# Kernel tuning notes

Measured on AMD Instinct MI355X. Metric: run time of the kernel, lower is better.

The kernel has to match this reference:

```python
import jax, jax.numpy as jnp
import numpy as np

N, L, D = 4, 2048, 1024
H_DIM, OUT_DIM = 1024, 1024


def setup_inputs() -> dict:
    key = jax.random.key(0)
    ks = jax.random.split(key, 7)
    scale = 0.02
    return {
        "x": jax.random.normal(ks[0], (N, L, D), dtype=jnp.float32),
        "Wq": jax.random.normal(ks[1], (D, H_DIM), dtype=jnp.float32) * scale,
        "bq": jnp.zeros((H_DIM,), dtype=jnp.float32),
        "Wk": jax.random.normal(ks[2], (D, H_DIM), dtype=jnp.float32) * scale,
        "bk": jnp.zeros((H_DIM,), dtype=jnp.float32),
        "Wv": jax.random.normal(ks[3], (D, OUT_DIM), dtype=jnp.float32) * scale,
        "bv": jnp.zeros((OUT_DIM,), dtype=jnp.float32),
    }


def reference(x, Wq, bq, Wk, bk, Wv, bv):
    # q,k: [N,L,h_dim], v: [N,L,out_dim]
    q = jnp.einsum("nld,dh->nlh", x, Wq) + bq
    k = jnp.einsum("nld,dh->nlh", x, Wk) + bk
    v = jnp.einsum("nld,do->nlo", x, Wv) + bv
    # scores: [N,L,L]
    qk = jnp.einsum("nlh,nmh->nlm", q, k)
    # NOTE: original scales by sqrt(qk.shape[-1]) == sqrt(L) (seq len), not sqrt(h_dim)
    seq_len = qk.shape[-1]
    s = jax.nn.softmax(qk / jnp.sqrt(jnp.asarray(seq_len, dtype=qk.dtype)), axis=-1)
    return jnp.einsum("nlm,nmo->nlo", s, v)
```

## Files before the change

### kernel.cpp

```cpp
#include <hip/hip_runtime.h>
#include <hip/hip_bf16.h>


typedef __attribute__((ext_vector_type(8))) short bf16x8;
typedef __attribute__((ext_vector_type(4))) float f32x4;

#define AS_G(p) ((__attribute__((address_space(1))) void*)(p))
#define AS_L(p) ((__attribute__((address_space(3))) void*)(p))

__device__ __forceinline__ unsigned short f2bf(float f) {
  unsigned int u = __float_as_uint(f);
  unsigned int lsb = (u >> 16) & 1u;
  u += 0x7fffu + lsb;
  return (unsigned short)(u >> 16);
}

#define WAITV(n) asm volatile("s_waitcnt vmcnt(" #n ")" ::: "memory")
#define BARRIER() do { asm volatile("" ::: "memory");                         \
    __builtin_amdgcn_s_barrier();                                             \
    asm volatile("" ::: "memory");                                            \
    __builtin_amdgcn_sched_barrier(0); } while (0)


#define S64A(ktk, rb, bofs)                                                   \
  __builtin_amdgcn_global_load_lds(                                           \
      AS_G(A + (size_t)(rowBase + (rb) * 64 + r0) * lda + (ktk) + goff),      \
      AS_L(lds + (bofs) + (rb) * 4096 + t * 8), 16, 0, 0)

#define S64B(ktk, rb, bofs)                                                   \
  __builtin_amdgcn_global_load_lds(                                           \
      AS_G(B + (size_t)(colBase + (rb) * 64 + r0) * ldb + (ktk) + goff),      \
      AS_L(lds + (bofs) + 16384 + (rb) * 4096 + t * 8), 16, 0, 0)

#define STAGE_TILE(ktk, bofs) do {                                            \
    S64A(ktk, 0, bofs); S64A(ktk, 1, bofs);                                   \
    S64A(ktk, 2, bofs); S64A(ktk, 3, bofs);                                   \
    S64B(ktk, 0, bofs); S64B(ktk, 1, bofs);                                   \
    S64B(ktk, 2, bofs); S64B(ktk, 3, bofs); } while (0)

#define LOAD_A(ih, bofs) do { _Pragma("unroll")                               \
    for (int ks_ = 0; ks_ < 2; ks_++) { _Pragma("unroll")                     \
      for (int ii = 0; ii < 4; ii++) {                                        \
        int row_ = wrow + ((ih) * 4 + ii) * 16 + r16;                         \
        int slot_ = (ks_ * 4 + q) ^ (r16 & 7);                                \
        af[ks_][ii] = *(const bf16x8*)(lds + (bofs) + row_ * 64 + slot_ * 8); \
      } } } while (0)

#define LOAD_B(jh, bofs) do { _Pragma("unroll")                               \
    for (int ks_ = 0; ks_ < 2; ks_++) { _Pragma("unroll")                     \
      for (int jj = 0; jj < 2; jj++) {                                        \
        int row_ = wcol + ((jh) * 2 + jj) * 16 + r16;                         \
        int slot_ = (ks_ * 4 + q) ^ (r16 & 7);                                \
        bfr[ks_][(jh) * 2 + jj] =                                             \
            *(const bf16x8*)(lds + (bofs) + 16384 + row_ * 64 + slot_ * 8);   \
      } } } while (0)

#define MM(ih, jh) do { __builtin_amdgcn_s_setprio(1); _Pragma("unroll")      \
    for (int ks_ = 0; ks_ < 2; ks_++) { _Pragma("unroll")                     \
      for (int ii = 0; ii < 4; ii++) { _Pragma("unroll")                      \
        for (int jj = 0; jj < 2; jj++)                                        \
          acc[(ih) * 4 + ii][(jh) * 2 + jj] =                                 \
              __builtin_amdgcn_mfma_f32_16x16x32_bf16(                        \
                  af[ks_][ii], bfr[ks_][(jh) * 2 + jj],                       \
                  acc[(ih) * 4 + ii][(jh) * 2 + jj], 0, 0, 0);                \
      } }                                                                     \
    __builtin_amdgcn_s_setprio(0); } while (0)

#define TILE(ktc, bofs, obofs) do {                                           \
                                                                      \
    LOAD_A(0, bofs); LOAD_B(0, bofs); LOAD_B(1, bofs);                        \
    if ((ktc) && (ktc) + 64 < K) {                                            \
      S64A((ktc) + 64, 1, obofs); S64A((ktc) + 64, 3, obofs);                 \
    }                                                                         \
    MM(0, 0); MM(0, 1);                                                       \
    BARRIER();                                                                \
                                                                      \
    LOAD_A(1, bofs);                                                          \
    if ((ktc) + 128 < K) {                                                    \
      S64A((ktc) + 128, 0, bofs); S64A((ktc) + 128, 2, bofs);                 \
      S64B((ktc) + 128, 0, bofs); S64B((ktc) + 128, 1, bofs);                 \
      S64B((ktc) + 128, 2, bofs); S64B((ktc) + 128, 3, bofs);                 \
    }                                                                         \
    MM(1, 1); MM(1, 0);                                                       \
    if ((ktc) + 128 < K) { WAITV(6); } else { WAITV(0); }                     \
    BARRIER(); } while (0)

template <int EPI>
__global__ __launch_bounds__(512, 2) void gemm_2r(
    const unsigned short* __restrict__ A, const unsigned short* __restrict__ B,
    float* __restrict__ Cf, long long sA, long long sB, long long sC,
    int K, int lda, int ldb, int ldc,
    unsigned short* __restrict__ u0, unsigned short* __restrict__ u1,
    unsigned short* __restrict__ u2,
    const float* __restrict__ f0, const float* __restrict__ f1,
    const float* __restrict__ f2,
    float* __restrict__ rsum, float scale)
{
  __shared__ unsigned short lds[2 * 32768];

  const int t = threadIdx.x;
  const int rowBase = blockIdx.y * 256;
  const int colBase = blockIdx.x * 256;
  A += (long long)blockIdx.z * sA;
  B += (long long)blockIdx.z * sB;

  const int l = t & 63;
  const int w = t >> 6;
  const int wrow = (w >> 2) * 128;
  const int wcol = (w & 3) * 64;
  const int q = l >> 4;
  const int r16 = l & 15;

  const int r0 = t >> 3;
  const int goff = ((t & 7) ^ (r0 & 7)) << 3;

  f32x4 acc[8][4] = {};
  bf16x8 af[2][4], bfr[2][4];

  STAGE_TILE(0, 0);
  STAGE_TILE(64, 32768);
  WAITV(8);
  BARRIER();

  for (int kt = 0; kt < K; kt += 128) {
    TILE(kt, 0, 32768);
    TILE(kt + 64, 32768, 0);
  }

  if (EPI == 1) {
    unsigned short* p16 = u0 + (long long)blockIdx.z * sC;
    float* rs = rsum + (long long)blockIdx.z * 2048;
#pragma unroll
    for (int i = 0; i < 8; i++) {
#pragma unroll
      for (int r = 0; r < 4; r++) {
        int row = rowBase + wrow + i * 16 + q * 4 + r;
        float rowpart = 0.f;
#pragma unroll
        for (int j = 0; j < 4; j++) {
          int col = colBase + wcol + j * 16 + r16;
          float e = __expf(acc[i][j][r] * scale);
          p16[(size_t)row * ldc + col] = f2bf(e);
          rowpart += e;
        }
#pragma unroll
        for (int m = 1; m < 16; m <<= 1) rowpart += __shfl_xor(rowpart, m);
        if (r16 == 0) atomicAdd(rs + row, rowpart);
      }
    }
  } else if (EPI == 2) {
    const int seg = colBase >> 10;
    if (seg < 2) {
      unsigned short* dst = seg ? u1 : u0;
      const float* bias = seg ? f1 : f0;
      const int cb = colBase & 1023;
#pragma unroll
      for (int i = 0; i < 8; i++) {
#pragma unroll
        for (int r = 0; r < 4; r++) {
          int row = rowBase + wrow + i * 16 + q * 4 + r;
#pragma unroll
          for (int j = 0; j < 4; j++) {
            int col = cb + wcol + j * 16 + r16;
            dst[(size_t)row * 1024 + col] = f2bf(acc[i][j][r] + bias[col]);
          }
        }
      }
    } else {
      const int ob = colBase - 2048;
#pragma unroll
      for (int i = 0; i < 8; i++) {
        int posBase = rowBase + wrow + i * 16 + q * 4;
        int b = posBase >> 11;
        int pos = posBase & 2047;
#pragma unroll
        for (int j = 0; j < 4; j++) {
          int o = ob + wcol + j * 16 + r16;
          float bias = f2[o];
          ushort4 pk;
          pk.x = f2bf(acc[i][j][0] + bias);
          pk.y = f2bf(acc[i][j][1] + bias);
          pk.z = f2bf(acc[i][j][2] + bias);
          pk.w = f2bf(acc[i][j][3] + bias);
          *(ushort4*)(u2 + ((size_t)((b << 10) + o) * 2048 + pos)) = pk;
        }
      }
    }
  } else {
    float* C = Cf + (long long)blockIdx.z * sC;
    const float* rs = rsum + (long long)blockIdx.z * 2048;
#pragma unroll
    for (int i = 0; i < 8; i++) {
#pragma unroll
      for (int r = 0; r < 4; r++) {
        int row = rowBase + wrow + i * 16 + q * 4 + r;
        float inv = 1.0f / rs[row];
#pragma unroll
        for (int j = 0; j < 4; j++) {
          int col = colBase + wcol + j * 16 + r16;
          C[(size_t)row * ldc + col] = acc[i][j][r] * inv;
        }
      }
    }
  }
}


__global__ __launch_bounds__(256) void cast_f32_to_bf16(
    const float* __restrict__ in, unsigned short* __restrict__ out, int n4,
    float* __restrict__ rzero, int nz4)
{
  int i = blockIdx.x * 256 + threadIdx.x;
  if (i < nz4) ((float4*)rzero)[i] = make_float4(0.f, 0.f, 0.f, 0.f);
  if (i >= n4) return;
  float4 v = ((const float4*)in)[i];
  ushort4 o;
  o.x = f2bf(v.x); o.y = f2bf(v.y); o.z = f2bf(v.z); o.w = f2bf(v.w);
  ((ushort4*)out)[i] = o;
}


__global__ __launch_bounds__(256) void wtrans(
    const float* __restrict__ Wq, const float* __restrict__ Wk,
    const float* __restrict__ Wv, unsigned short* __restrict__ WT)
{
  __shared__ float tile[32][33];
  const float* in = blockIdx.z == 0 ? Wq : (blockIdx.z == 1 ? Wk : Wv);
  unsigned short* out = WT + (size_t)blockIdx.z * 1024 * 1024;
  const int bc = blockIdx.x * 32;
  const int br = blockIdx.y * 32;
  const int tx = threadIdx.x;
  const int ty = threadIdx.y;
#pragma unroll
  for (int i = 0; i < 4; i++)
    tile[ty + i * 8][tx] = in[(size_t)(br + ty + i * 8) * 1024 + bc + tx];
  __syncthreads();
#pragma unroll
  for (int i = 0; i < 4; i++)
    out[(size_t)(bc + ty + i * 8) * 1024 + br + tx] = f2bf(tile[tx][ty + i * 8]);
}


extern "C" void kernel_launch(void* const* d_in, const int* in_sizes, int n_in,
                              void* d_out, int out_size, void* d_ws, size_t ws_size,
                              hipStream_t stream) {
  (void)in_sizes; (void)n_in; (void)out_size;

  const float* x  = (const float*)d_in[0];
  const float* Wq = (const float*)d_in[1];
  const float* bq = (const float*)d_in[2];
  const float* Wk = (const float*)d_in[3];
  const float* bk = (const float*)d_in[4];
  const float* Wv = (const float*)d_in[5];
  const float* bv = (const float*)d_in[6];
  float* out = (float*)d_out;

  const int Nb = 4, L = 2048, D = 1024, H = 1024, O = 1024;
  const int M = Nb * L;
  const int NQKV = 3 * H;

  char* ws = (char*)d_ws;
  size_t off = 0;
  unsigned short* xb = (unsigned short*)(ws + off); off += (size_t)M * D * 2;
  unsigned short* qb = (unsigned short*)(ws + off); off += (size_t)M * H * 2;
  unsigned short* kb = (unsigned short*)(ws + off); off += (size_t)M * H * 2;
  unsigned short* vt = (unsigned short*)(ws + off); off += (size_t)M * O * 2;
  unsigned short* WT = (unsigned short*)(ws + off); off += (size_t)NQKV * D * 2;
  unsigned short* P  = (unsigned short*)(ws + off); off += (size_t)Nb * L * L * 2;
  float* rsum = (float*)(ws + off); off += (size_t)Nb * L * 4;
  if (ws_size < off) return;

  dim3 blk256(256);
  dim3 blk512(512);

  cast_f32_to_bf16<<<(M * D / 4 + 255) / 256, blk256, 0, stream>>>(
      x, xb, M * D / 4, rsum, Nb * L / 4);

  wtrans<<<dim3(32, 32, 3), dim3(32, 8), 0, stream>>>(Wq, Wk, Wv, WT);

  gemm_2r<2><<<dim3(NQKV / 256, M / 256, 1), blk512, 0, stream>>>(
      xb, WT, nullptr, 0, 0, 0, D, D, D, 0,
      qb, kb, vt, bq, bk, bv, nullptr, 0.f);

  gemm_2r<1><<<dim3(L / 256, L / 256, Nb), blk512, 0, stream>>>(
      qb, kb, nullptr, (long long)L * H, (long long)L * H, (long long)L * L,
      H, H, H, L,
      P, nullptr, nullptr, nullptr, nullptr, nullptr,
      rsum, 0.022097086912079608f );

  gemm_2r<3><<<dim3(O / 256, L / 256, Nb), blk512, 0, stream>>>(
      P, vt, out, (long long)L * L, (long long)O * L, (long long)L * O,
      L, L, L, O,
      nullptr, nullptr, nullptr, nullptr, nullptr, nullptr,
      rsum, 0.f);
}
```

Before: 253.0 us.

## Shrink GEMM tiles to 128x128 with 256-thread blocks and restaged pipeline

```diff
diff --git a/kernel.cpp b/kernel.cpp
--- a/kernel.cpp
+++ b/kernel.cpp
@@ -16,77 +16,69 @@
 }
 
 #define WAITV(n) asm volatile("s_waitcnt vmcnt(" #n ")" ::: "memory")
-#define BARRIER() do { asm volatile("" ::: "memory");                         \
+#define BAR() do { asm volatile("" ::: "memory");                             \
     __builtin_amdgcn_s_barrier();                                             \
-    asm volatile("" ::: "memory");                                            \
-    __builtin_amdgcn_sched_barrier(0); } while (0)
-
-
-#define S64A(ktk, rb, bofs)                                                   \
+    asm volatile("" ::: "memory"); } while (0)
+
+
+#define BUFE 16384
+
+#define S32A(ktk, rb, bofs)                                                   \
   __builtin_amdgcn_global_load_lds(                                           \
-      AS_G(A + (size_t)(rowBase + (rb) * 64 + r0) * lda + (ktk) + goff),      \
-      AS_L(lds + (bofs) + (rb) * 4096 + t * 8), 16, 0, 0)
-
-#define S64B(ktk, rb, bofs)                                                   \
+      AS_G(A + (size_t)(rowBase + (rb) * 32 + r0) * lda + (ktk) + goff),      \
+      AS_L(lds + (bofs) + (rb) * 2048 + t * 8), 16, 0, 0)
+
+#define S32B(ktk, rb, bofs)                                                   \
   __builtin_amdgcn_global_load_lds(                                           \
-      AS_G(B + (size_t)(colBase + (rb) * 64 + r0) * ldb + (ktk) + goff),      \
-      AS_L(lds + (bofs) + 16384 + (rb) * 4096 + t * 8), 16, 0, 0)
-
-#define STAGE_TILE(ktk, bofs) do {                                            \
-    S64A(ktk, 0, bofs); S64A(ktk, 1, bofs);                                   \
-    S64A(ktk, 2, bofs); S64A(ktk, 3, bofs);                                   \
-    S64B(ktk, 0, bofs); S64B(ktk, 1, bofs);                                   \
-    S64B(ktk, 2, bofs); S64B(ktk, 3, bofs); } while (0)
-
-#define LOAD_A(ih, bofs) do { _Pragma("unroll")                               \
+      AS_G(B + (size_t)(colBase + (rb) * 32 + r0) * ldb + (ktk) + goff),      \
+      AS_L(lds + (bofs) + 8192 + (rb) * 2048 + t * 8), 16, 0, 0)
+
+#define LDA4(bofs) do { _Pragma("unroll")                                     \
     for (int ks_ = 0; ks_ < 2; ks_++) { _Pragma("unroll")                     \
       for (int ii = 0; ii < 4; ii++) {                                        \
-        int row_ = wrow + ((ih) * 4 + ii) * 16 + r16;                         \
+        int row_ = wrow + ii * 16 + r16;                                      \
         int slot_ = (ks_ * 4 + q) ^ (r16 & 7);                                \
         af[ks_][ii] = *(const bf16x8*)(lds + (bofs) + row_ * 64 + slot_ * 8); \
       } } } while (0)
 
-#define LOAD_B(jh, bofs) do { _Pragma("unroll")                               \
+#define LDB(jh, bofs) do { _Pragma("unroll")                                  \
     for (int ks_ = 0; ks_ < 2; ks_++) { _Pragma("unroll")                     \
       for (int jj = 0; jj < 2; jj++) {                                        \
         int row_ = wcol + ((jh) * 2 + jj) * 16 + r16;                         \
         int slot_ = (ks_ * 4 + q) ^ (r16 & 7);                                \
         bfr[ks_][(jh) * 2 + jj] =                                             \
-            *(const bf16x8*)(lds + (bofs) + 16384 + row_ * 64 + slot_ * 8);   \
+            *(const bf16x8*)(lds + (bofs) + 8192 + row_ * 64 + slot_ * 8);    \
       } } } while (0)
 
-#define MM(ih, jh) do { __builtin_amdgcn_s_setprio(1); _Pragma("unroll")      \
+#define MMQ(j0, j1) do { __builtin_amdgcn_s_setprio(1); _Pragma("unroll")     \
     for (int ks_ = 0; ks_ < 2; ks_++) { _Pragma("unroll")                     \
       for (int ii = 0; ii < 4; ii++) { _Pragma("unroll")                      \
-        for (int jj = 0; jj < 2; jj++)                                        \
-          acc[(ih) * 4 + ii][(jh) * 2 + jj] =                                 \
-              __builtin_amdgcn_mfma_f32_16x16x32_bf16(                        \
-                  af[ks_][ii], bfr[ks_][(jh) * 2 + jj],                       \
-                  acc[(ih) * 4 + ii][(jh) * 2 + jj], 0, 0, 0);                \
+        for (int jj = (j0); jj <= (j1); jj++)                                 \
+          acc[ii][jj] = __builtin_amdgcn_mfma_f32_16x16x32_bf16(              \
+              af[ks_][ii], bfr[ks_][jj], acc[ii][jj], 0, 0, 0);               \
       } }                                                                     \
     __builtin_amdgcn_s_setprio(0); } while (0)
 
 #define TILE(ktc, bofs, obofs) do {                                           \
-                                                                      \
-    LOAD_A(0, bofs); LOAD_B(0, bofs); LOAD_B(1, bofs);                        \
+                      \
+    LDA4(bofs); LDB(0, bofs);                                                 \
     if ((ktc) && (ktc) + 64 < K) {                                            \
-      S64A((ktc) + 64, 1, obofs); S64A((ktc) + 64, 3, obofs);                 \
+      S32B((ktc) + 64, 0, obofs); S32B((ktc) + 64, 1, obofs);                 \
+      S32B((ktc) + 64, 2, obofs); S32B((ktc) + 64, 3, obofs);                 \
     }                                                                         \
-    MM(0, 0); MM(0, 1);                                                       \
-    BARRIER();                                                                \
-                                                                      \
-    LOAD_A(1, bofs);                                                          \
+    BAR(); MMQ(0, 1); BAR();                                                  \
+                  \
+    LDB(1, bofs);                                                             \
     if ((ktc) + 128 < K) {                                                    \
-      S64A((ktc) + 128, 0, bofs); S64A((ktc) + 128, 2, bofs);                 \
-      S64B((ktc) + 128, 0, bofs); S64B((ktc) + 128, 1, bofs);                 \
-      S64B((ktc) + 128, 2, bofs); S64B((ktc) + 128, 3, bofs);                 \
+      S32A((ktc) + 128, 0, bofs); S32A((ktc) + 128, 1, bofs);                 \
+      S32A((ktc) + 128, 2, bofs); S32A((ktc) + 128, 3, bofs);                 \
     }                                                                         \
-    MM(1, 1); MM(1, 0);                                                       \
-    if ((ktc) + 128 < K) { WAITV(6); } else { WAITV(0); }                     \
-    BARRIER(); } while (0)
+    BAR(); MMQ(2, 3);                                                         \
+    if ((ktc) + 128 < K) { WAITV(4); } else { WAITV(0); }                     \
+    BAR(); } while (0)
 
 template <int EPI>
-__global__ __launch_bounds__(512, 2) void gemm_2r(
+__global__ __launch_bounds__(256, 2) void gemm_db(
     const unsigned short* __restrict__ A, const unsigned short* __restrict__ B,
     float* __restrict__ Cf, long long sA, long long sB, long long sC,
     int K, int lda, int ldb, int ldc,
@@ -96,42 +88,44 @@
     const float* __restrict__ f2,
     float* __restrict__ rsum, float scale)
 {
-  __shared__ unsigned short lds[2 * 32768];
+  __shared__ unsigned short lds[2 * BUFE];
 
   const int t = threadIdx.x;
-  const int rowBase = blockIdx.y * 256;
-  const int colBase = blockIdx.x * 256;
+  const int rowBase = blockIdx.y * 128;
+  const int colBase = blockIdx.x * 128;
   A += (long long)blockIdx.z * sA;
   B += (long long)blockIdx.z * sB;
 
   const int l = t & 63;
   const int w = t >> 6;
-  const int wrow = (w >> 2) * 128;
-  const int wcol = (w & 3) * 64;
+  const int wrow = (w >> 1) * 64;
+  const int wcol = (w & 1) * 64;
   const int q = l >> 4;
   const int r16 = l & 15;
 
   const int r0 = t >> 3;
   const int goff = ((t & 7) ^ (r0 & 7)) << 3;
 
-  f32x4 acc[8][4] = {};
+  f32x4 acc[4][4] = {};
   bf16x8 af[2][4], bfr[2][4];
 
-  STAGE_TILE(0, 0);
-  STAGE_TILE(64, 32768);
+  S32A(0, 0, 0); S32A(0, 1, 0); S32A(0, 2, 0); S32A(0, 3, 0);
+  S32B(0, 0, 0); S32B(0, 1, 0); S32B(0, 2, 0); S32B(0, 3, 0);
+  S32A(64, 0, BUFE); S32A(64, 1, BUFE); S32A(64, 2, BUFE); S32A(64, 3, BUFE);
+  S32B(64, 0, BUFE); S32B(64, 1, BUFE); S32B(64, 2, BUFE); S32B(64, 3, BUFE);
   WAITV(8);
-  BARRIER();
+  BAR();
 
   for (int kt = 0; kt < K; kt += 128) {
-    TILE(kt, 0, 32768);
-    TILE(kt + 64, 32768, 0);
+    TILE(kt, 0, BUFE);
+    TILE(kt + 64, BUFE, 0);
   }
 
   if (EPI == 1) {
     unsigned short* p16 = u0 + (long long)blockIdx.z * sC;
     float* rs = rsum + (long long)blockIdx.z * 2048;
 #pragma unroll
-    for (int i = 0; i < 8; i++) {
+    for (int i = 0; i < 4; i++) {
 #pragma unroll
       for (int r = 0; r < 4; r++) {
         int row = rowBase + wrow + i * 16 + q * 4 + r;
@@ -155,7 +149,7 @@
       const float* bias = seg ? f1 : f0;
       const int cb = colBase & 1023;
 #pragma unroll
-      for (int i = 0; i < 8; i++) {
+      for (int i = 0; i < 4; i++) {
 #pragma unroll
         for (int r = 0; r < 4; r++) {
           int row = rowBase + wrow + i * 16 + q * 4 + r;
@@ -169,7 +163,7 @@
     } else {
       const int ob = colBase - 2048;
 #pragma unroll
-      for (int i = 0; i < 8; i++) {
+      for (int i = 0; i < 4; i++) {
         int posBase = rowBase + wrow + i * 16 + q * 4;
         int b = posBase >> 11;
         int pos = posBase & 2047;
@@ -190,7 +184,7 @@
     float* C = Cf + (long long)blockIdx.z * sC;
     const float* rs = rsum + (long long)blockIdx.z * 2048;
 #pragma unroll
-    for (int i = 0; i < 8; i++) {
+    for (int i = 0; i < 4; i++) {
 #pragma unroll
       for (int r = 0; r < 4; r++) {
         int row = rowBase + wrow + i * 16 + q * 4 + r;
@@ -271,24 +265,23 @@
   if (ws_size < off) return;
 
   dim3 blk256(256);
-  dim3 blk512(512);
 
   cast_f32_to_bf16<<<(M * D / 4 + 255) / 256, blk256, 0, stream>>>(
       x, xb, M * D / 4, rsum, Nb * L / 4);
 
   wtrans<<<dim3(32, 32, 3), dim3(32, 8), 0, stream>>>(Wq, Wk, Wv, WT);
 
-  gemm_2r<2><<<dim3(NQKV / 256, M / 256, 1), blk512, 0, stream>>>(
+  gemm_db<2><<<dim3(NQKV / 128, M / 128, 1), blk256, 0, stream>>>(
       xb, WT, nullptr, 0, 0, 0, D, D, D, 0,
       qb, kb, vt, bq, bk, bv, nullptr, 0.f);
 
-  gemm_2r<1><<<dim3(L / 256, L / 256, Nb), blk512, 0, stream>>>(
+  gemm_db<1><<<dim3(L / 128, L / 128, Nb), blk256, 0, stream>>>(
       qb, kb, nullptr, (long long)L * H, (long long)L * H, (long long)L * L,
       H, H, H, L,
       P, nullptr, nullptr, nullptr, nullptr, nullptr,
       rsum, 0.022097086912079608f );
 
-  gemm_2r<3><<<dim3(O / 256, L / 256, Nb), blk512, 0, stream>>>(
+  gemm_db<3><<<dim3(O / 128, L / 128, Nb), blk256, 0, stream>>>(
       P, vt, out, (long long)L * L, (long long)O * L, (long long)L * O,
       L, L, L, O,
       nullptr, nullptr, nullptr, nullptr, nullptr, nullptr,
```

After: 240.5 us. 5.0% less time.
